# Kernel tuning notes

Measured on AMD Instinct MI355X. Metric: run time of the kernel, lower is better.

## Reference

```python
import jax, jax.numpy as jnp
import numpy as np

TOPK = 6
E = 512
IN = 384
M = 8192
LN_EPS = 1e-5


def _lin(x, w, b):
    # torch nn.Linear: y = x @ W^T + b, W is [out, in]
    return x @ w.T + b


def setup_inputs() -> dict:
    key = jax.random.key(0)
    ks = jax.random.split(key, 16)
    s = lambda k, sh: (jax.random.normal(k, sh, dtype=jnp.float32) * 0.02)
    return {
        "x": jax.random.normal(ks[0], (1, M, IN), dtype=jnp.float32),
        "fc1_w": s(ks[1], (E, IN)), "fc1_b": jnp.zeros((E,), jnp.float32),
        "wh_w": s(ks[2], (E, E)),   "wh_b": jnp.zeros((E,), jnp.float32),
        "wt_w": s(ks[3], (E, E)),   "wt_b": jnp.zeros((E,), jnp.float32),
        "l1_w": s(ks[4], (E, E)),   "l1_b": jnp.zeros((E,), jnp.float32),
        "l2_w": s(ks[5], (E, E)),   "l2_b": jnp.zeros((E,), jnp.float32),
        "a1_w": s(ks[6], (E // 2, E)), "a1_b": jnp.zeros((E // 2,), jnp.float32),
        "a2_w": s(ks[7], (1, E // 2)), "a2_b": jnp.zeros((1,), jnp.float32),
        "ln_g": jnp.ones((E,), jnp.float32), "ln_b": jnp.zeros((E,), jnp.float32),
    }


def reference(x, fc1_w, fc1_b, wh_w, wh_b, wt_w, wt_b,
              l1_w, l1_b, l2_w, l2_b, a1_w, a1_b, a2_w, a2_b, ln_g, ln_b):
    lrelu = jax.nn.leaky_relu  # slope 0.01 == torch default
    h = lrelu(_lin(x, fc1_w, fc1_b))                      # [B,M,E]
    h = (h + h.mean(axis=1, keepdims=True)) * 0.5
    e_h = _lin(h, wh_w, wh_b)                             # [B,M,E]
    e_t = _lin(h, wt_w, wt_b)                             # [B,M,E]
    scale = E ** (-0.5)
    attn_logit = (e_h * scale) @ jnp.swapaxes(e_t, -2, -1)  # [B,M,M]
    topk_weight, topk_index = jax.lax.top_k(attn_logit, TOPK)  # [B,M,K]
    # gather top-k neighbor tail embeddings: [B,M,K,E]
    Nb_h = jax.vmap(lambda et, idx: et[idx])(e_t, topk_index)
    topk_prob = jax.nn.softmax(topk_weight, axis=2)       # [B,M,K]
    eh_r = topk_prob[..., None] * Nb_h + (1.0 - topk_prob)[..., None] * e_h[:, :, None, :]
    gate = jnp.tanh(e_h[:, :, None, :] + eh_r)            # [B,M,K,E]
    # faithful to torch einsum('ijkl,ijkm->ijk'): sums l and m independently
    ka_weight = Nb_h.sum(axis=-1) * gate.sum(axis=-1)     # [B,M,K]
    ka_prob = jax.nn.softmax(ka_weight, axis=2)           # [B,M,K]
    e_Nh = jnp.einsum('bmk,bmke->bme', ka_prob, Nb_h)     # [B,M,E]
    sum_emb = lrelu(_lin(e_h + e_Nh, l1_w, l1_b))
    bi_emb = lrelu(_lin(e_h * e_Nh, l2_w, l2_b))
    emb = sum_emb + bi_emb                                # [B,M,E] (dropout = eval identity)
    hn = emb[0]                                           # squeeze(0) -> [M,E]
    # GeoGlobalAttention readout: gate_nn = Linear->LeakyReLU->Linear, softmax over nodes
    g = _lin(lrelu(_lin(hn, a1_w, a1_b)), a2_w, a2_b)     # [M,1]
    att = jax.nn.softmax(g, axis=0)
    pooled = (att * hn).sum(axis=0, keepdims=True)        # [1,E]
    mu = pooled.mean(axis=-1, keepdims=True)
    var = jnp.mean((pooled - mu) ** 2, axis=-1, keepdims=True)
    out = (pooled - mu) / jnp.sqrt(var + LN_EPS) * ln_g + ln_b
    return out
```

## Files before the change

### kernel.cpp

```cpp
#include <hip/hip_runtime.h>
#include <math.h>
#include <stdint.h>

#define M_NODES 8192
#define E_DIM   512
#define NTOPK   6
#define ATTN_SCALE 0.04419417382415922f
#define NEG_BIG (-1e38f)
#define CAND_CAP 192

typedef __attribute__((ext_vector_type(8))) short short8;
typedef __attribute__((ext_vector_type(4))) float f32x4;

__device__ __forceinline__ float lrelu(float v) { return v > 0.f ? v : 0.01f * v; }

__device__ __forceinline__ unsigned short f2bf(float f) {
  uint32_t u = __float_as_uint(f);
  uint32_t r = (u + 0x7FFFu + ((u >> 16) & 1u)) >> 16;
  return (unsigned short)r;
}
__device__ __forceinline__ float bf2f(unsigned short s) {
  return __uint_as_float(((uint32_t)s) << 16);
}

__device__ __forceinline__ void async_cp16(const void* gptr, void* lds) {
  auto g1 = reinterpret_cast<const __attribute__((address_space(1))) unsigned int*>(
      reinterpret_cast<uintptr_t>(gptr));
  auto l3 = reinterpret_cast<__attribute__((address_space(3))) unsigned int*>(
      reinterpret_cast<uintptr_t>(lds));
  __builtin_amdgcn_global_load_lds(g1, l3, 16, 0, 0);
}



__global__ __launch_bounds__(256) void wcast_kernel(
    const float* __restrict__ x, const float* __restrict__ fc1w,
    const float* __restrict__ whw, const float* __restrict__ wtw,
    const float* __restrict__ l1w, const float* __restrict__ l2w,
    const float* __restrict__ a1w,
    unsigned short* __restrict__ xT, unsigned short* __restrict__ fc1T,
    unsigned short* __restrict__ whT, unsigned short* __restrict__ wtT,
    unsigned short* __restrict__ l1T, unsigned short* __restrict__ l2T,
    unsigned short* __restrict__ a1T)
{
  const int gid = blockIdx.x * 256 + threadIdx.x;
  const float* src; unsigned short* dst; int K8, local;
  if (gid < 417792) {
    K8 = 48;
    if (gid < 393216) { src = x; dst = xT; local = gid; }
    else { src = fc1w; dst = fc1T; local = gid - 393216; }
  } else {
    K8 = 64;
    if (gid < 450560)      { src = whw; dst = whT; local = gid - 417792; }
    else if (gid < 483328) { src = wtw; dst = wtT; local = gid - 450560; }
    else if (gid < 516096) { src = l1w; dst = l1T; local = gid - 483328; }
    else if (gid < 548864) { src = l2w; dst = l2T; local = gid - 516096; }
    else                   { src = a1w; dst = a1T; local = gid - 548864; }
  }
  const int m = local / K8;
  const int k8 = local - m * K8;
  const float* p = src + (size_t)m * (K8 * 8) + k8 * 8;
  float4 v0 = ((const float4*)p)[0];
  float4 v1 = ((const float4*)p)[1];
  const int Kt = K8 >> 2;
  const size_t ti = ((size_t)(m >> 4) * Kt + (k8 >> 2)) * 512 + ((m & 15) + 16 * (k8 & 3)) * 8;
  uint4 pk;
  pk.x = (uint32_t)f2bf(v0.x) | ((uint32_t)f2bf(v0.y) << 16);
  pk.y = (uint32_t)f2bf(v0.z) | ((uint32_t)f2bf(v0.w) << 16);
  pk.z = (uint32_t)f2bf(v1.x) | ((uint32_t)f2bf(v1.y) << 16);
  pk.w = (uint32_t)f2bf(v1.z) | ((uint32_t)f2bf(v1.w) << 16);
  *(uint4*)(dst + ti) = pk;
}

__global__ __launch_bounds__(256, 4) void gemm1_kernel(
    const unsigned short* __restrict__ xT, const unsigned short* __restrict__ fc1T,
    const float* __restrict__ b1, unsigned short* __restrict__ hT,
    float* __restrict__ colsum)
{
  __shared__ unsigned short As[8 * 512];
  __shared__ unsigned short Bs[8 * 512];
  const int tid = threadIdx.x, lane = tid & 63, w = tid >> 6;
  const int wr = w >> 1, wc = w & 1;
  const int m0 = blockIdx.y * 128;
  const int n0 = blockIdx.x * 128;

  f32x4 acc[4][4];
#pragma unroll
  for (int i = 0; i < 4; i++)
#pragma unroll
    for (int j = 0; j < 4; j++) acc[i][j] = (f32x4){0.f, 0.f, 0.f, 0.f};

  for (int kt = 0; kt < 12; kt++) {
    const int s0 = w, s1 = w + 4;
    async_cp16(xT + ((size_t)((m0 >> 4) + s0) * 12 + kt) * 512 + lane * 8, &As[s0 * 512]);
    async_cp16(xT + ((size_t)((m0 >> 4) + s1) * 12 + kt) * 512 + lane * 8, &As[s1 * 512]);
    async_cp16(fc1T + ((size_t)((n0 >> 4) + s0) * 12 + kt) * 512 + lane * 8, &Bs[s0 * 512]);
    async_cp16(fc1T + ((size_t)((n0 >> 4) + s1) * 12 + kt) * 512 + lane * 8, &Bs[s1 * 512]);
    __syncthreads();
    short8 a[4], b[4];
#pragma unroll
    for (int i = 0; i < 4; i++) a[i] = *(const short8*)&As[(wr * 4 + i) * 512 + lane * 8];
#pragma unroll
    for (int j = 0; j < 4; j++) b[j] = *(const short8*)&Bs[(wc * 4 + j) * 512 + lane * 8];
#pragma unroll
    for (int i = 0; i < 4; i++)
#pragma unroll
      for (int j = 0; j < 4; j++)
        acc[i][j] = __builtin_amdgcn_mfma_f32_16x16x32_bf16(a[i], b[j], acc[i][j], 0, 0, 0);
    __syncthreads();
  }

  const int q = lane >> 4, lcol = lane & 15;
  float colp[4] = {};
#pragma unroll
  for (int i = 0; i < 4; i++)
#pragma unroll
    for (int j = 0; j < 4; j++) {
      const int c = n0 + wc * 64 + j * 16 + lcol;
      const float bias = b1[c];
#pragma unroll
      for (int d = 0; d < 4; d++) {
        const int r = m0 + wr * 64 + i * 16 + q * 4 + d;
        const float v = 0.5f * lrelu(acc[i][j][d] + bias);
        hT[((size_t)(r >> 4) * 16 + (c >> 5)) * 512 +
           ((r & 15) + 16 * ((c >> 3) & 3)) * 8 + (c & 7)] = f2bf(v);
        colp[j] += v;
      }
    }
#pragma unroll
  for (int j = 0; j < 4; j++) {
    colp[j] += __shfl_xor(colp[j], 16);
    colp[j] += __shfl_xor(colp[j], 32);
  }
  if (lane < 16) {
#pragma unroll
    for (int j = 0; j < 4; j++)
      atomicAdd(&colsum[n0 + wc * 64 + j * 16 + lcol], colp[j]);
  }
}

__global__ __launch_bounds__(256) void meanproj_kernel(
    const float* __restrict__ colsum, const float* __restrict__ whw,
    const float* __restrict__ wtw, const float* __restrict__ whb,
    const float* __restrict__ wtb, float* __restrict__ biasHT)
{
  const int lane = threadIdx.x & 63;
  const int c1024 = blockIdx.x * 4 + (threadIdx.x >> 6);
  const bool isH = c1024 < 512;
  const int c = isH ? c1024 : c1024 - 512;
  const float* W = (isH ? whw : wtw) + (size_t)c * 512 + lane * 8;
  const float* cs = colsum + lane * 8;
  float s = 0.f;
#pragma unroll
  for (int e = 0; e < 8; e++) s = fmaf(cs[e], W[e], s);
#pragma unroll
  for (int off = 32; off; off >>= 1) s += __shfl_xor(s, off);
  if (lane == 0)
    biasHT[c1024] = (isH ? whb : wtb)[c] + s * (1.f / (float)M_NODES);
}

__global__ __launch_bounds__(256, 4) void dual_gemm(
    const unsigned short* __restrict__ hT, const unsigned short* __restrict__ wstackT,
    const float* __restrict__ biasHT,
    unsigned short* __restrict__ ehT, unsigned short* __restrict__ etT,
    unsigned short* __restrict__ ehRow, unsigned short* __restrict__ etRow)
{
  __shared__ unsigned short As[8 * 512];
  __shared__ unsigned short Bs[8 * 512];
  const int tid = threadIdx.x, lane = tid & 63, w = tid >> 6;
  const int wr = w >> 1, wc = w & 1;
  const int m0 = blockIdx.y * 128;
  const int n0 = blockIdx.x * 128;

  f32x4 acc[4][4];
#pragma unroll
  for (int i = 0; i < 4; i++)
#pragma unroll
    for (int j = 0; j < 4; j++) acc[i][j] = (f32x4){0.f, 0.f, 0.f, 0.f};

  for (int kt = 0; kt < 16; kt++) {
    const int s0 = w, s1 = w + 4;
    async_cp16(hT + ((size_t)((m0 >> 4) + s0) * 16 + kt) * 512 + lane * 8, &As[s0 * 512]);
    async_cp16(hT + ((size_t)((m0 >> 4) + s1) * 16 + kt) * 512 + lane * 8, &As[s1 * 512]);
    async_cp16(wstackT + ((size_t)((n0 >> 4) + s0) * 16 + kt) * 512 + lane * 8, &Bs[s0 * 512]);
    async_cp16(wstackT + ((size_t)((n0 >> 4) + s1) * 16 + kt) * 512 + lane * 8, &Bs[s1 * 512]);
    __syncthreads();
    short8 a[4], b[4];
#pragma unroll
    for (int i = 0; i < 4; i++) a[i] = *(const short8*)&As[(wr * 4 + i) * 512 + lane * 8];
#pragma unroll
    for (int j = 0; j < 4; j++) b[j] = *(const short8*)&Bs[(wc * 4 + j) * 512 + lane * 8];
#pragma unroll
    for (int i = 0; i < 4; i++)
#pragma unroll
      for (int j = 0; j < 4; j++)
        acc[i][j] = __builtin_amdgcn_mfma_f32_16x16x32_bf16(a[i], b[j], acc[i][j], 0, 0, 0);
    __syncthreads();
  }

  const int q = lane >> 4, lcol = lane & 15;
  const bool isH = (n0 < 512);
  const int cb = isH ? n0 : (n0 - 512);
  unsigned short* T = isH ? ehT : etT;
  unsigned short* R = isH ? ehRow : etRow;

#pragma unroll
  for (int i = 0; i < 4; i++)
#pragma unroll
    for (int j = 0; j < 4; j++) {
      const int cl = wc * 64 + j * 16 + lcol;
      const float bias = biasHT[n0 + cl];
      const int c = cb + cl;
#pragma unroll
      for (int d = 0; d < 4; d++) {
        const int r = m0 + wr * 64 + i * 16 + q * 4 + d;
        const unsigned short us = f2bf(acc[i][j][d] + bias);
        T[((size_t)(r >> 4) * 16 + (c >> 5)) * 512 +
          ((r & 15) + 16 * ((c >> 3) & 3)) * 8 + (c & 7)] = us;
        R[(size_t)r * E_DIM + c] = us;
      }
    }
}

template <int MODE>
__global__ __launch_bounds__(256) void mfma_gemm(
    const unsigned short* __restrict__ At1, const unsigned short* __restrict__ At2,
    const unsigned short* __restrict__ Wt1, const unsigned short* __restrict__ Wt2,
    const float* __restrict__ b1, const float* __restrict__ b2,
    float* __restrict__ Cf, unsigned short* __restrict__ T1,
    unsigned short* __restrict__ Cbf, int N, int K)
{
  constexpr bool DUALW = (MODE == 2);
  __shared__ unsigned short As[2][8 * 512];
  __shared__ unsigned short Bs[2][4 * 512];
  const int Kt = K >> 5;
  const int tid = threadIdx.x, lane = tid & 63, w = tid >> 6;
  const int m0 = blockIdx.y * 128, n0 = blockIdx.x * 64;

  f32x4 acc0[2][4], acc1[2][4];
#pragma unroll
  for (int p = 0; p < 2; p++)
#pragma unroll
    for (int j = 0; j < 4; j++) {
      acc0[p][j] = (f32x4){0.f, 0.f, 0.f, 0.f};
      acc1[p][j] = (f32x4){0.f, 0.f, 0.f, 0.f};
    }

  for (int kt = 0; kt < Kt; kt++) {
    const unsigned short* a1p = At1 + ((size_t)((m0 >> 4) + 2 * w) * Kt + kt) * 512 + lane * 8;
    async_cp16(a1p, &As[0][(2 * w) * 512]);
    async_cp16(a1p + (size_t)Kt * 512, &As[0][(2 * w + 1) * 512]);
    if (MODE == 2) {
      const unsigned short* a2p = At2 + ((size_t)((m0 >> 4) + 2 * w) * Kt + kt) * 512 + lane * 8;
      async_cp16(a2p, &As[1][(2 * w) * 512]);
      async_cp16(a2p + (size_t)Kt * 512, &As[1][(2 * w + 1) * 512]);
    }
    const unsigned short* bp1 = Wt1 + ((size_t)((n0 >> 4) + w) * Kt + kt) * 512 + lane * 8;
    async_cp16(bp1, &Bs[0][w * 512]);
    if (DUALW) {
      const unsigned short* bp2 = Wt2 + ((size_t)((n0 >> 4) + w) * Kt + kt) * 512 + lane * 8;
      async_cp16(bp2, &Bs[1][w * 512]);
    }
    __syncthreads();
    short8 a[2], a2[2], bb[4], bb2[4];
#pragma unroll
    for (int p = 0; p < 2; p++) a[p] = *(const short8*)&As[0][(2 * w + p) * 512 + lane * 8];
    if (MODE == 2) {
#pragma unroll
      for (int p = 0; p < 2; p++) a2[p] = *(const short8*)&As[1][(2 * w + p) * 512 + lane * 8];
    }
#pragma unroll
    for (int j = 0; j < 4; j++) bb[j] = *(const short8*)&Bs[0][j * 512 + lane * 8];
    if (DUALW) {
#pragma unroll
      for (int j = 0; j < 4; j++) bb2[j] = *(const short8*)&Bs[1][j * 512 + lane * 8];
    }
#pragma unroll
    for (int p = 0; p < 2; p++)
#pragma unroll
      for (int j = 0; j < 4; j++) {
        acc0[p][j] = __builtin_amdgcn_mfma_f32_16x16x32_bf16(a[p], bb[j], acc0[p][j], 0, 0, 0);
        if (MODE == 2)
          acc1[p][j] = __builtin_amdgcn_mfma_f32_16x16x32_bf16(a2[p], bb2[j], acc1[p][j], 0, 0, 0);
      }
    __syncthreads();
  }

  const int lrow = (lane >> 4) * 4, lcol = lane & 15;

  if (MODE == 3) {
    float part[2][4] = {};
#pragma unroll
    for (int p = 0; p < 2; p++)
#pragma unroll
      for (int j = 0; j < 4; j++) {
        const int c = n0 + j * 16 + lcol;
        const float bias1 = b1[c];
        const float w2 = b2[c];
#pragma unroll
        for (int d = 0; d < 4; d++)
          part[p][d] = fmaf(lrelu(acc0[p][j][d] + bias1), w2, part[p][d]);
      }
#pragma unroll
    for (int p = 0; p < 2; p++)
#pragma unroll
      for (int d = 0; d < 4; d++) {
#pragma unroll
        for (int off = 1; off < 16; off <<= 1)
          part[p][d] += __shfl_xor(part[p][d], off);
      }
    if (lcol == 0) {
#pragma unroll
      for (int p = 0; p < 2; p++)
#pragma unroll
        for (int d = 0; d < 4; d++)
          atomicAdd(&Cf[m0 + w * 32 + p * 16 + lrow + d], part[p][d]);
    }
    return;
  }

  const int NT = N >> 5;
#pragma unroll
  for (int p = 0; p < 2; p++)
#pragma unroll
    for (int j = 0; j < 4; j++) {
      const int c = n0 + j * 16 + lcol;
      const float bias1 = b1[c];
      const float bias2 = b2[c];
#pragma unroll
      for (int d = 0; d < 4; d++) {
        const int r = m0 + w * 32 + p * 16 + lrow + d;
        const float e = lrelu(acc0[p][j][d] + bias1) + lrelu(acc1[p][j][d] + bias2);
        T1[((size_t)(r >> 4) * NT + (c >> 5)) * 512 +
           ((r & 15) + 16 * ((c >> 3) & 3)) * 8 + (c & 7)] = f2bf(e);
        Cbf[(size_t)r * N + c] = f2bf(e);
      }
    }
}

__global__ __launch_bounds__(256, 4) void sgemm_kernel(
    const unsigned short* __restrict__ ehT, const unsigned short* __restrict__ etT,
    unsigned short* __restrict__ sc, float* __restrict__ tmax)
{
  __shared__ unsigned short As[8 * 512];
  __shared__ unsigned short Bs[8 * 512];
  const int tid = threadIdx.x, lane = tid & 63, w = tid >> 6;
  const int wr = w >> 1, wc = w & 1;
  const int m0 = blockIdx.y * 128;
  const int n0 = blockIdx.x * 128;

  f32x4 acc[4][4];
#pragma unroll
  for (int i = 0; i < 4; i++)
#pragma unroll
    for (int j = 0; j < 4; j++) acc[i][j] = (f32x4){0.f, 0.f, 0.f, 0.f};

  for (int kt = 0; kt < 16; kt++) {
    const int s0 = w, s1 = w + 4;
    async_cp16(ehT + ((size_t)((m0 >> 4) + s0) * 16 + kt) * 512 + lane * 8, &As[s0 * 512]);
    async_cp16(ehT + ((size_t)((m0 >> 4) + s1) * 16 + kt) * 512 + lane * 8, &As[s1 * 512]);
    async_cp16(etT + ((size_t)((n0 >> 4) + s0) * 16 + kt) * 512 + lane * 8, &Bs[s0 * 512]);
    async_cp16(etT + ((size_t)((n0 >> 4) + s1) * 16 + kt) * 512 + lane * 8, &Bs[s1 * 512]);
    __syncthreads();
    short8 a[4], b[4];
#pragma unroll
    for (int i = 0; i < 4; i++) a[i] = *(const short8*)&As[(wr * 4 + i) * 512 + lane * 8];
#pragma unroll
    for (int j = 0; j < 4; j++) b[j] = *(const short8*)&Bs[(wc * 4 + j) * 512 + lane * 8];
#pragma unroll
    for (int i = 0; i < 4; i++)
#pragma unroll
      for (int j = 0; j < 4; j++)
        acc[i][j] = __builtin_amdgcn_mfma_f32_16x16x32_bf16(a[i], b[j], acc[i][j], 0, 0, 0);
    __syncthreads();
  }

  const int q = lane >> 4, lcol = lane & 15;
  const int bn = blockIdx.x;

  float rm[4][4];
#pragma unroll
  for (int i = 0; i < 4; i++)
#pragma unroll
    for (int d = 0; d < 4; d++) rm[i][d] = NEG_BIG;

#pragma unroll
  for (int i = 0; i < 4; i++)
#pragma unroll
    for (int d = 0; d < 4; d++) {
      unsigned short o[4];
#pragma unroll
      for (int j = 0; j < 4; j++) {
        o[j] = f2bf(acc[i][j][d]);
        rm[i][d] = fmaxf(rm[i][d], bf2f(o[j]));
      }
      const int row = m0 + wr * 64 + i * 16 + q * 4 + d;
      const size_t off = ((size_t)row * 64 + bn) * 128 + (wc * 16 + lcol) * 4;
      *(uint2*)(sc + off) = *(uint2*)o;
    }

#pragma unroll
  for (int i = 0; i < 4; i++)
#pragma unroll
    for (int d = 0; d < 4; d++) {
#pragma unroll
      for (int off = 1; off < 16; off <<= 1)
        rm[i][d] = fmaxf(rm[i][d], __shfl_xor(rm[i][d], off));
    }

  if (lcol == 0) {
#pragma unroll
    for (int i = 0; i < 4; i++)
#pragma unroll
      for (int d = 0; d < 4; d++)
        tmax[(size_t)(m0 + wr * 64 + i * 16 + q * 4 + d) * 128 +
             bn * 2 + wc] = rm[i][d];
  }
}

__global__ __launch_bounds__(256) void scan_combine_kernel(
    const unsigned short* __restrict__ sc, const float* __restrict__ tmax,
    const unsigned short* __restrict__ ehRow, const unsigned short* __restrict__ etRow,
    unsigned short* __restrict__ s1T, unsigned short* __restrict__ s2T)
{
  __shared__ float cv[4][CAND_CAP];
  __shared__ int   ci[4][CAND_CAP];
  __shared__ int   cnt[4];
  __shared__ float t6v[4][8];
  __shared__ int   t6i[4][8];
  const int tid = threadIdx.x;
  const int lane = tid & 63;
  const int w = tid >> 6;
  const int row = blockIdx.x * 4 + w;

  if (lane == 0) cnt[w] = 0;
  if (lane < 8) { t6v[w][lane] = 0.f; t6i[w][lane] = 0; }

  const float* tm = tmax + (size_t)row * 128;
  const float v2 = fmaxf(tm[lane], tm[lane + 64]);
  const float bmax = fmaxf(tm[2 * lane], tm[2 * lane + 1]);
  uint32_t u = __float_as_uint(v2);
  u = ((int)u >= 0) ? (u | 0x80000000u) : ~u;
  uint32_t key = (u & ~63u) | (uint32_t)lane;
  float tau = 0.f;
#pragma unroll
  for (int it = 0; it < 6; it++) {
    uint32_t k = key;
#pragma unroll
    for (int off = 32; off; off >>= 1) {
      const uint32_t o = (uint32_t)__shfl_xor((int)k, off);
      k = k > o ? k : o;
    }
    const int wl = (int)(k & 63u);
    if (it == 5) tau = __shfl(v2, wl);
    if (lane == wl) key = 0u;
  }

  unsigned long long mask = __ballot(bmax >= tau);
  const unsigned short* rp = sc + (size_t)row * 8192;
  while (mask) {
    const int bn = __ffsll(mask) - 1;
    mask &= mask - 1;
    const uint32_t uu = *(const uint32_t*)(rp + bn * 128 + lane * 2);
    const float f0 = bf2f((unsigned short)(uu & 0xFFFFu));
    const float f1 = bf2f((unsigned short)(uu >> 16));
#pragma unroll
    for (int e = 0; e < 2; e++) {
      const float f = e ? f1 : f0;
      if (f >= tau) {
        const int idx128 = lane * 2 + e;
        const int g = idx128 >> 2, j = idx128 & 3;
        const int col = bn * 128 + (g >> 4) * 64 + j * 16 + (g & 15);
        const int slot = atomicAdd(&cnt[w], 1);
        if (slot < CAND_CAP) { cv[w][slot] = f; ci[w][slot] = col; }
      }
    }
  }
  __syncthreads();

  int n = cnt[w];
  n = n < CAND_CAP ? n : CAND_CAP;
  for (int c = lane; c < n; c += 64) {
    const float v = cv[w][c];
    const int idx = ci[w][c];
    int rank = 0;
    for (int j = 0; j < n; j++) {
      const float vj = cv[w][j];
      rank += (vj > v) || (vj == v && ci[w][j] < idx);
    }
    if (rank < NTOPK) { t6v[w][rank] = v; t6i[w][rank] = idx; }
  }
  __syncthreads();

  const int m = row;
  float wv[NTOPK]; int id[NTOPK];
#pragma unroll
  for (int k = 0; k < NTOPK; k++) {
    wv[k] = t6v[w][k] * ATTN_SCALE;
    id[k] = t6i[w][k];
  }

  float mx = wv[0];
#pragma unroll
  for (int k = 1; k < NTOPK; k++) mx = fmaxf(mx, wv[k]);
  float p[NTOPK]; float s = 0.f;
#pragma unroll
  for (int k = 0; k < NTOPK; k++) { p[k] = expf(wv[k] - mx); s += p[k]; }
  const float inv = 1.f / s;
#pragma unroll
  for (int k = 0; k < NTOPK; k++) p[k] *= inv;

  short8 eh8 = *(const short8*)(ehRow + (size_t)m * E_DIM + lane * 8);
  float ehv[8];
#pragma unroll
  for (int e = 0; e < 8; e++) ehv[e] = bf2f((unsigned short)eh8[e]);

  float nv[NTOPK][8];
#pragma unroll
  for (int k = 0; k < NTOPK; k++) {
    short8 nb = *(const short8*)(etRow + (size_t)id[k] * E_DIM + lane * 8);
#pragma unroll
    for (int e = 0; e < 8; e++) nv[k][e] = bf2f((unsigned short)nb[e]);
  }

  float ka[NTOPK];
#pragma unroll
  for (int k = 0; k < NTOPK; k++) {
    float snb = 0.f, sg = 0.f;
    const float aa = 2.f - p[k], bb = p[k];
#pragma unroll
    for (int e = 0; e < 8; e++) {
      snb += nv[k][e];
      sg += tanhf(fmaf(aa, ehv[e], bb * nv[k][e]));
    }
#pragma unroll
    for (int off = 32; off; off >>= 1) {
      snb += __shfl_xor(snb, off);
      sg += __shfl_xor(sg, off);
    }
    ka[k] = snb * sg;
  }
  float km = ka[0];
#pragma unroll
  for (int k = 1; k < NTOPK; k++) km = fmaxf(km, ka[k]);
  float kp[NTOPK]; float ks = 0.f;
#pragma unroll
  for (int k = 0; k < NTOPK; k++) { kp[k] = expf(ka[k] - km); ks += kp[k]; }
  const float kinv = 1.f / ks;

  const size_t tbase = ((size_t)(m >> 4) * 16 + (lane >> 2)) * 512 +
                       ((m & 15) + 16 * (lane & 3)) * 8;
  unsigned short o1[8], o2[8];
#pragma unroll
  for (int e = 0; e < 8; e++) {
    float o = 0.f;
#pragma unroll
    for (int k = 0; k < NTOPK; k++) o = fmaf(kp[k], nv[k][e], o);
    o *= kinv;
    o1[e] = f2bf(ehv[e] + o);
    o2[e] = f2bf(ehv[e] * o);
  }
  *(short8*)(s1T + tbase) = *(short8*)o1;
  *(short8*)(s2T + tbase) = *(short8*)o2;
}

__global__ __launch_bounds__(256) void pooled_kernel(
    const unsigned short* __restrict__ emb, const float* __restrict__ g,
    float* __restrict__ pooled, float* __restrict__ wsum)
{
  const int t = threadIdx.x;
  const int r0 = blockIdx.x * 128;
  float a0 = 0.f, a1 = 0.f, lsum = 0.f;
  for (int r = 0; r < 128; r++) {
    const int m = r0 + r;
    const float wv = expf(g[m]);
    lsum += wv;
    a0 = fmaf(wv, bf2f(emb[(size_t)m * E_DIM + t]), a0);
    a1 = fmaf(wv, bf2f(emb[(size_t)m * E_DIM + 256 + t]), a1);
  }
  atomicAdd(&pooled[t], a0);
  atomicAdd(&pooled[t + 256], a1);
  if (t == 0) atomicAdd(wsum, lsum);
}

__global__ __launch_bounds__(512) void ln_kernel(
    const float* __restrict__ pooled, const float* __restrict__ wsum,
    const float* __restrict__ lng, const float* __restrict__ lnb,
    float* __restrict__ out)
{
  __shared__ float red[8];
  __shared__ float red2[8];
  const int t = threadIdx.x;
  const float v = pooled[t] / wsum[0];
  float s = v;
#pragma unroll
  for (int off = 32; off; off >>= 1) s += __shfl_xor(s, off);
  if ((t & 63) == 0) red[t >> 6] = s;
  __syncthreads();
  float tot = 0.f;
  for (int i = 0; i < 8; i++) tot += red[i];
  const float mu = tot / (float)E_DIM;
  const float d = v - mu;
  float q = d * d;
#pragma unroll
  for (int off = 32; off; off >>= 1) q += __shfl_xor(q, off);
  if ((t & 63) == 0) red2[t >> 6] = q;
  __syncthreads();
  float vt = 0.f;
  for (int i = 0; i < 8; i++) vt += red2[i];
  const float var = vt / (float)E_DIM;
  out[t] = d * rsqrtf(var + 1e-5f) * lng[t] + lnb[t];
}

extern "C" void kernel_launch(void* const* d_in, const int* in_sizes, int n_in,
                              void* d_out, int out_size, void* d_ws, size_t ws_size,
                              hipStream_t stream)
{
  const float* x     = (const float*)d_in[0];
  const float* fc1_w = (const float*)d_in[1];
  const float* fc1_b = (const float*)d_in[2];
  const float* wh_w  = (const float*)d_in[3];
  const float* wh_b  = (const float*)d_in[4];
  const float* wt_w  = (const float*)d_in[5];
  const float* wt_b  = (const float*)d_in[6];
  const float* l1_w  = (const float*)d_in[7];
  const float* l1_b  = (const float*)d_in[8];
  const float* l2_w  = (const float*)d_in[9];
  const float* l2_b  = (const float*)d_in[10];
  const float* a1_w  = (const float*)d_in[11];
  const float* a1_b  = (const float*)d_in[12];
  const float* a2_w  = (const float*)d_in[13];
  const float* a2_b  = (const float*)d_in[14];
  const float* ln_g  = (const float*)d_in[15];
  const float* ln_b  = (const float*)d_in[16];
  (void)a2_b;

  char* ws = (char*)d_ws;
  const size_t MiB = 1 << 20;
  unsigned short* fc1T = (unsigned short*)(ws + 0);
  unsigned short* whT  = (unsigned short*)(ws + 393216);
  unsigned short* wtT  = (unsigned short*)(ws + 917504);
  unsigned short* l1T  = (unsigned short*)(ws + 1441792);
  unsigned short* l2T  = (unsigned short*)(ws + 1966080);
  unsigned short* a1T  = (unsigned short*)(ws + 2490368);
  unsigned short* xT     = (unsigned short*)(ws + 3 * MiB);
  unsigned short* hT     = (unsigned short*)(ws + 25 * MiB);
  unsigned short* ehT    = (unsigned short*)(ws + 33 * MiB);
  unsigned short* etT    = (unsigned short*)(ws + 41 * MiB);
  unsigned short* ehRow  = (unsigned short*)(ws + 49 * MiB);
  unsigned short* etRow  = (unsigned short*)(ws + 57 * MiB);
  float*          tmaxb  = (float*)(ws + 65 * MiB);
  unsigned short* s1T    = (unsigned short*)(ws + 3 * MiB);
  unsigned short* s2T    = (unsigned short*)(ws + 11 * MiB);
  unsigned short* embT   = (unsigned short*)(ws + 19 * MiB);
  unsigned short* embRow = (unsigned short*)(ws + 27 * MiB);
  unsigned short* scores = (unsigned short*)(ws + 96 * MiB);
  char*           smal   = ws + 69 * MiB;
  float* colsum = (float*)(smal);
  float* biasHT = (float*)(smal + 2048);
  float* g      = (float*)(smal + 8192);
  float* stats  = (float*)(smal + 40960);
  float* pooled = (float*)(smal + 45056);

  hipMemsetAsync(smal, 0, 47104, stream);

  wcast_kernel<<<2208, 256, 0, stream>>>(x, fc1_w, wh_w, wt_w, l1_w, l2_w, a1_w,
                                         xT, fc1T, whT, wtT, l1T, l2T, a1T);
  gemm1_kernel<<<dim3(4, 64), 256, 0, stream>>>(xT, fc1T, fc1_b, hT, colsum);
  meanproj_kernel<<<256, 256, 0, stream>>>(colsum, wh_w, wt_w, wh_b, wt_b, biasHT);
  dual_gemm<<<dim3(8, 64), 256, 0, stream>>>(hT, whT, biasHT, ehT, etT, ehRow, etRow);
  sgemm_kernel<<<dim3(64, 64), 256, 0, stream>>>(ehT, etT, scores, tmaxb);
  scan_combine_kernel<<<M_NODES / 4, 256, 0, stream>>>(
      scores, tmaxb, ehRow, etRow, s1T, s2T);
  mfma_gemm<2><<<dim3(8, 64), 256, 0, stream>>>(
      s1T, s2T, l1T, l2T, l1_b, l2_b, nullptr, embT, embRow, 512, 512);
  mfma_gemm<3><<<dim3(4, 64), 256, 0, stream>>>(
      embT, nullptr, a1T, nullptr, a1_b, a2_w, g, nullptr, nullptr, 256, 512);
  pooled_kernel<<<64, 256, 0, stream>>>(embRow, g, pooled, stats);
  ln_kernel<<<1, 512, 0, stream>>>(pooled, stats, ln_g, ln_b, (float*)d_out);
}
```

Before: 296.5 us.

## Enlarge score GEMM tile to 256x256 with double-buffered LDS and setprio

The M×M score GEMM now uses 256x256 block tiles with 8 waves instead of 128x128 with 4 waves, and a K step of 64 rather than 32. The next K-tile is prefetched asynchronously into a second LDS buffer while the current one is consumed. The MFMA issue is split into quadrant phases, each wrapped in s_setprio and separated by barriers. The aim is to reduce global and LDS traffic per FLOP and hide load latency, at the cost of higher register and LDS use (128 KB per block), which limits occupancy.

```diff
diff --git a/kernel.cpp b/kernel.cpp
--- a/kernel.cpp
+++ b/kernel.cpp
@@ -338,83 +338,147 @@
     }
 }
 
-__global__ __launch_bounds__(256, 4) void sgemm_kernel(
+__global__ __launch_bounds__(512, 2) void sgemm_kernel(
     const unsigned short* __restrict__ ehT, const unsigned short* __restrict__ etT,
     unsigned short* __restrict__ sc, float* __restrict__ tmax)
 {
-  __shared__ unsigned short As[8 * 512];
-  __shared__ unsigned short Bs[8 * 512];
+  __shared__ unsigned short As[2][32 * 512];
+  __shared__ unsigned short Bs[2][32 * 512];
   const int tid = threadIdx.x, lane = tid & 63, w = tid >> 6;
-  const int wr = w >> 1, wc = w & 1;
-  const int m0 = blockIdx.y * 128;
-  const int n0 = blockIdx.x * 128;
-
-  f32x4 acc[4][4];
-#pragma unroll
-  for (int i = 0; i < 4; i++)
+  const int wr = w >> 2, wc = w & 3;
+  const int m0 = blockIdx.y * 256;
+  const int n0 = blockIdx.x * 256;
+
+  f32x4 acc[8][4];
+#pragma unroll
+  for (int i = 0; i < 8; i++)
 #pragma unroll
     for (int j = 0; j < 4; j++) acc[i][j] = (f32x4){0.f, 0.f, 0.f, 0.f};
 
-  for (int kt = 0; kt < 16; kt++) {
-    const int s0 = w, s1 = w + 4;
-    async_cp16(ehT + ((size_t)((m0 >> 4) + s0) * 16 + kt) * 512 + lane * 8, &As[s0 * 512]);
-    async_cp16(ehT + ((size_t)((m0 >> 4) + s1) * 16 + kt) * 512 + lane * 8, &As[s1 * 512]);
-    async_cp16(etT + ((size_t)((n0 >> 4) + s0) * 16 + kt) * 512 + lane * 8, &Bs[s0 * 512]);
-    async_cp16(etT + ((size_t)((n0 >> 4) + s1) * 16 + kt) * 512 + lane * 8, &Bs[s1 * 512]);
+  auto stage = [&](int kt, int bsel) {
+#pragma unroll
+    for (int r = 0; r < 8; r++) {
+      const int c = r * 8 + w;
+      if (c < 32) {
+        async_cp16(ehT + ((size_t)((m0 >> 4) + (c >> 1)) * 16 + (kt * 2 + (c & 1))) * 512 + lane * 8,
+                   &As[bsel][c * 512]);
+      } else {
+        const int c2 = c - 32;
+        async_cp16(etT + ((size_t)((n0 >> 4) + (c2 >> 1)) * 16 + (kt * 2 + (c2 & 1))) * 512 + lane * 8,
+                   &Bs[bsel][c2 * 512]);
+      }
+    }
+  };
+
+  stage(0, 0);
+
+  short8 af[8], bf[8];
+  for (int kt = 0; kt < 8; kt++) {
+    const int cur = kt & 1;
     __syncthreads();
-    short8 a[4], b[4];
-#pragma unroll
-    for (int i = 0; i < 4; i++) a[i] = *(const short8*)&As[(wr * 4 + i) * 512 + lane * 8];
-#pragma unroll
-    for (int j = 0; j < 4; j++) b[j] = *(const short8*)&Bs[(wc * 4 + j) * 512 + lane * 8];
-#pragma unroll
-    for (int i = 0; i < 4; i++)
-#pragma unroll
-      for (int j = 0; j < 4; j++)
-        acc[i][j] = __builtin_amdgcn_mfma_f32_16x16x32_bf16(a[i], b[j], acc[i][j], 0, 0, 0);
-    __syncthreads();
+    if (kt < 7) stage(kt + 1, cur ^ 1);
+
+#pragma unroll
+    for (int ii = 0; ii < 4; ii++)
+#pragma unroll
+      for (int ks = 0; ks < 2; ks++)
+        af[ii * 2 + ks] = *(const short8*)&As[cur][((wr * 8 + ii) * 2 + ks) * 512 + lane * 8];
+#pragma unroll
+    for (int jj = 0; jj < 2; jj++)
+#pragma unroll
+      for (int ks = 0; ks < 2; ks++)
+        bf[jj * 2 + ks] = *(const short8*)&Bs[cur][((wc * 4 + jj) * 2 + ks) * 512 + lane * 8];
+    __builtin_amdgcn_s_setprio(1);
+#pragma unroll
+    for (int ii = 0; ii < 4; ii++)
+#pragma unroll
+      for (int jj = 0; jj < 2; jj++)
+#pragma unroll
+        for (int ks = 0; ks < 2; ks++)
+          acc[ii][jj] = __builtin_amdgcn_mfma_f32_16x16x32_bf16(
+              af[ii * 2 + ks], bf[jj * 2 + ks], acc[ii][jj], 0, 0, 0);
+    __builtin_amdgcn_s_setprio(0);
+    __builtin_amdgcn_s_barrier();
+
+#pragma unroll
+    for (int jj = 2; jj < 4; jj++)
+#pragma unroll
+      for (int ks = 0; ks < 2; ks++)
+        bf[jj * 2 + ks] = *(const short8*)&Bs[cur][((wc * 4 + jj) * 2 + ks) * 512 + lane * 8];
+    __builtin_amdgcn_s_setprio(1);
+#pragma unroll
+    for (int ii = 0; ii < 4; ii++)
+#pragma unroll
+      for (int jj = 2; jj < 4; jj++)
+#pragma unroll
+        for (int ks = 0; ks < 2; ks++)
+          acc[ii][jj] = __builtin_amdgcn_mfma_f32_16x16x32_bf16(
+              af[ii * 2 + ks], bf[jj * 2 + ks], acc[ii][jj], 0, 0, 0);
+    __builtin_amdgcn_s_setprio(0);
+    __builtin_amdgcn_s_barrier();
+
+#pragma unroll
+    for (int ii = 0; ii < 4; ii++)
+#pragma unroll
+      for (int ks = 0; ks < 2; ks++)
+        af[ii * 2 + ks] = *(const short8*)&As[cur][((wr * 8 + 4 + ii) * 2 + ks) * 512 + lane * 8];
+    __builtin_amdgcn_s_setprio(1);
+#pragma unroll
+    for (int ii = 0; ii < 4; ii++)
+#pragma unroll
+      for (int jj = 2; jj < 4; jj++)
+#pragma unroll
+        for (int ks = 0; ks < 2; ks++)
+          acc[4 + ii][jj] = __builtin_amdgcn_mfma_f32_16x16x32_bf16(
+              af[ii * 2 + ks], bf[jj * 2 + ks], acc[4 + ii][jj], 0, 0, 0);
+    __builtin_amdgcn_s_setprio(0);
+    __builtin_amdgcn_s_barrier();
+
+    __builtin_amdgcn_s_setprio(1);
+#pragma unroll
+    for (int ii = 0; ii < 4; ii++)
+#pragma unroll
+      for (int jj = 0; jj < 2; jj++)
+#pragma unroll
+        for (int ks = 0; ks < 2; ks++)
+          acc[4 + ii][jj] = __builtin_amdgcn_mfma_f32_16x16x32_bf16(
+              af[ii * 2 + ks], bf[jj * 2 + ks], acc[4 + ii][jj], 0, 0, 0);
+    __builtin_amdgcn_s_setprio(0);
   }
 
   const int q = lane >> 4, lcol = lane & 15;
-  const int bn = blockIdx.x;
-
-  float rm[4][4];
-#pragma unroll
-  for (int i = 0; i < 4; i++)
-#pragma unroll
-    for (int d = 0; d < 4; d++) rm[i][d] = NEG_BIG;
-
-#pragma unroll
-  for (int i = 0; i < 4; i++)
+  const int bn = blockIdx.x * 2 + (wc >> 1);
+  const int wcS = wc & 1;
+
+#pragma unroll
+  for (int i = 0; i < 8; i++) {
+    float rm[4];
+#pragma unroll
+    for (int d = 0; d < 4; d++) rm[d] = NEG_BIG;
 #pragma unroll
     for (int d = 0; d < 4; d++) {
       unsigned short o[4];
 #pragma unroll
       for (int j = 0; j < 4; j++) {
         o[j] = f2bf(acc[i][j][d]);
-        rm[i][d] = fmaxf(rm[i][d], bf2f(o[j]));
-      }
-      const int row = m0 + wr * 64 + i * 16 + q * 4 + d;
-      const size_t off = ((size_t)row * 64 + bn) * 128 + (wc * 16 + lcol) * 4;
+        rm[d] = fmaxf(rm[d], bf2f(o[j]));
+      }
+      const int row = m0 + wr * 128 + i * 16 + q * 4 + d;
+      const size_t off = ((size_t)row * 64 + bn) * 128 + (wcS * 16 + lcol) * 4;
       *(uint2*)(sc + off) = *(uint2*)o;
     }
-
-#pragma unroll
-  for (int i = 0; i < 4; i++)
 #pragma unroll
     for (int d = 0; d < 4; d++) {
 #pragma unroll
-      for (int off = 1; off < 16; off <<= 1)
-        rm[i][d] = fmaxf(rm[i][d], __shfl_xor(rm[i][d], off));
-    }
-
-  if (lcol == 0) {
-#pragma unroll
-    for (int i = 0; i < 4; i++)
+      for (int off2 = 1; off2 < 16; off2 <<= 1)
+        rm[d] = fmaxf(rm[d], __shfl_xor(rm[d], off2));
+    }
+    if (lcol == 0) {
 #pragma unroll
       for (int d = 0; d < 4; d++)
-        tmax[(size_t)(m0 + wr * 64 + i * 16 + q * 4 + d) * 128 +
-             bn * 2 + wc] = rm[i][d];
+        tmax[(size_t)(m0 + wr * 128 + i * 16 + q * 4 + d) * 128 +
+             blockIdx.x * 4 + wc] = rm[d];
+    }
   }
 }
 
@@ -669,7 +733,7 @@
   gemm1_kernel<<<dim3(4, 64), 256, 0, stream>>>(xT, fc1T, fc1_b, hT, colsum);
   meanproj_kernel<<<256, 256, 0, stream>>>(colsum, wh_w, wt_w, wh_b, wt_b, biasHT);
   dual_gemm<<<dim3(8, 64), 256, 0, stream>>>(hT, whT, biasHT, ehT, etT, ehRow, etRow);
-  sgemm_kernel<<<dim3(64, 64), 256, 0, stream>>>(ehT, etT, scores, tmaxb);
+  sgemm_kernel<<<dim3(32, 32), 512, 0, stream>>>(ehT, etT, scores, tmaxb);
   scan_combine_kernel<<<M_NODES / 4, 256, 0, stream>>>(
       scores, tmaxb, ehRow, etRow, s1T, s2T);
   mfma_gemm<2><<<dim3(8, 64), 256, 0, stream>>>(
```

New measurement: 299.2 us. No clear change (+0.9%).

## Compute per-segment top-6 in score GEMM epilogue instead of writing full scores

Applied to the files above, without the earlier changes.

The score GEMM epilogue no longer writes the full 8192x8192 bf16 score matrix and per-tile maxima. Each 64-column segment now reduces to its top-6 packed keys (order-preserving bf16 value plus inverted column index) with wave shuffles, and stores only those. The combine kernel merges the 128 sorted segment lists per row with a wave-wide argmax loop, replacing the threshold scan, LDS candidate buffer and rank sort. This removes about 128 MB of score traffic, at the cost of six shuffle-reduction rounds per output row in the GEMM epilogue.

```diff
diff --git a/kernel.cpp b/kernel.cpp
--- a/kernel.cpp
+++ b/kernel.cpp
@@ -6,8 +6,7 @@
 #define E_DIM   512
 #define NTOPK   6
 #define ATTN_SCALE 0.04419417382415922f
-#define NEG_BIG (-1e38f)
-#define CAND_CAP 192
+#define CAND_SEGS 128
 
 typedef __attribute__((ext_vector_type(8))) short short8;
 typedef __attribute__((ext_vector_type(4))) float f32x4;
@@ -340,7 +339,7 @@
 
 __global__ __launch_bounds__(256, 4) void sgemm_kernel(
     const unsigned short* __restrict__ ehT, const unsigned short* __restrict__ etT,
-    unsigned short* __restrict__ sc, float* __restrict__ tmax)
+    uint32_t* __restrict__ cand)
 {
   __shared__ unsigned short As[8 * 512];
   __shared__ unsigned short Bs[8 * 512];
@@ -376,128 +375,86 @@
   }
 
   const int q = lane >> 4, lcol = lane & 15;
-  const int bn = blockIdx.x;
-
-  float rm[4][4];
+  const int seg = blockIdx.x * 2 + wc;
+
 #pragma unroll
   for (int i = 0; i < 4; i++)
 #pragma unroll
-    for (int d = 0; d < 4; d++) rm[i][d] = NEG_BIG;
-
-#pragma unroll
-  for (int i = 0; i < 4; i++)
-#pragma unroll
     for (int d = 0; d < 4; d++) {
-      unsigned short o[4];
+      uint32_t kb[4];
 #pragma unroll
       for (int j = 0; j < 4; j++) {
-        o[j] = f2bf(acc[i][j][d]);
-        rm[i][d] = fmaxf(rm[i][d], bf2f(o[j]));
-      }
-      const int row = m0 + wr * 64 + i * 16 + q * 4 + d;
-      const size_t off = ((size_t)row * 64 + bn) * 128 + (wc * 16 + lcol) * 4;
-      *(uint2*)(sc + off) = *(uint2*)o;
-    }
-
-#pragma unroll
-  for (int i = 0; i < 4; i++)
-#pragma unroll
-    for (int d = 0; d < 4; d++) {
-#pragma unroll
-      for (int off = 1; off < 16; off <<= 1)
-        rm[i][d] = fmaxf(rm[i][d], __shfl_xor(rm[i][d], off));
-    }
-
-  if (lcol == 0) {
-#pragma unroll
-    for (int i = 0; i < 4; i++)
-#pragma unroll
-      for (int d = 0; d < 4; d++)
-        tmax[(size_t)(m0 + wr * 64 + i * 16 + q * 4 + d) * 128 +
-             bn * 2 + wc] = rm[i][d];
-  }
-}
-
-__global__ __launch_bounds__(256) void scan_combine_kernel(
-    const unsigned short* __restrict__ sc, const float* __restrict__ tmax,
+        const int col = n0 + wc * 64 + j * 16 + lcol;
+        const uint32_t ub = ((uint32_t)f2bf(acc[i][j][d])) << 16;
+        const uint32_t ob = ((int)ub >= 0) ? (ub | 0x80000000u) : ~ub;
+        kb[j] = (ob & 0xFFFF0000u) | (uint32_t)(8191 - col);
+      }
+      uint32_t sel[6];
+#pragma unroll
+      for (int t = 0; t < 6; t++) {
+        uint32_t m01 = kb[0] > kb[1] ? kb[0] : kb[1];
+        uint32_t m23 = kb[2] > kb[3] ? kb[2] : kb[3];
+        uint32_t m = m01 > m23 ? m01 : m23;
+#pragma unroll
+        for (int off = 1; off < 16; off <<= 1) {
+          const uint32_t o = (uint32_t)__shfl_xor((int)m, off);
+          m = m > o ? m : o;
+        }
+        sel[t] = m;
+#pragma unroll
+        for (int j = 0; j < 4; j++)
+          if (kb[j] == m) kb[j] = 0u;
+      }
+      if (lcol == 0) {
+        const int row = m0 + wr * 64 + i * 16 + q * 4 + d;
+        uint32_t* cp = cand + ((size_t)row * CAND_SEGS + seg) * 6;
+        uint2 u01; u01.x = sel[0]; u01.y = sel[1];
+        uint2 u23; u23.x = sel[2]; u23.y = sel[3];
+        uint2 u45; u45.x = sel[4]; u45.y = sel[5];
+        ((uint2*)cp)[0] = u01;
+        ((uint2*)cp)[1] = u23;
+        ((uint2*)cp)[2] = u45;
+      }
+    }
+}
+
+__global__ __launch_bounds__(256) void combine_kernel(
+    const uint32_t* __restrict__ cand,
     const unsigned short* __restrict__ ehRow, const unsigned short* __restrict__ etRow,
     unsigned short* __restrict__ s1T, unsigned short* __restrict__ s2T)
 {
-  __shared__ float cv[4][CAND_CAP];
-  __shared__ int   ci[4][CAND_CAP];
-  __shared__ int   cnt[4];
-  __shared__ float t6v[4][8];
-  __shared__ int   t6i[4][8];
   const int tid = threadIdx.x;
   const int lane = tid & 63;
   const int w = tid >> 6;
   const int row = blockIdx.x * 4 + w;
-
-  if (lane == 0) cnt[w] = 0;
-  if (lane < 8) { t6v[w][lane] = 0.f; t6i[w][lane] = 0; }
-
-  const float* tm = tmax + (size_t)row * 128;
-  const float v2 = fmaxf(tm[lane], tm[lane + 64]);
-  const float bmax = fmaxf(tm[2 * lane], tm[2 * lane + 1]);
-  uint32_t u = __float_as_uint(v2);
-  u = ((int)u >= 0) ? (u | 0x80000000u) : ~u;
-  uint32_t key = (u & ~63u) | (uint32_t)lane;
-  float tau = 0.f;
-#pragma unroll
-  for (int it = 0; it < 6; it++) {
-    uint32_t k = key;
-#pragma unroll
-    for (int off = 32; off; off >>= 1) {
-      const uint32_t o = (uint32_t)__shfl_xor((int)k, off);
-      k = k > o ? k : o;
-    }
-    const int wl = (int)(k & 63u);
-    if (it == 5) tau = __shfl(v2, wl);
-    if (lane == wl) key = 0u;
-  }
-
-  unsigned long long mask = __ballot(bmax >= tau);
-  const unsigned short* rp = sc + (size_t)row * 8192;
-  while (mask) {
-    const int bn = __ffsll(mask) - 1;
-    mask &= mask - 1;
-    const uint32_t uu = *(const uint32_t*)(rp + bn * 128 + lane * 2);
-    const float f0 = bf2f((unsigned short)(uu & 0xFFFFu));
-    const float f1 = bf2f((unsigned short)(uu >> 16));
-#pragma unroll
-    for (int e = 0; e < 2; e++) {
-      const float f = e ? f1 : f0;
-      if (f >= tau) {
-        const int idx128 = lane * 2 + e;
-        const int g = idx128 >> 2, j = idx128 & 3;
-        const int col = bn * 128 + (g >> 4) * 64 + j * 16 + (g & 15);
-        const int slot = atomicAdd(&cnt[w], 1);
-        if (slot < CAND_CAP) { cv[w][slot] = f; ci[w][slot] = col; }
-      }
-    }
-  }
-  __syncthreads();
-
-  int n = cnt[w];
-  n = n < CAND_CAP ? n : CAND_CAP;
-  for (int c = lane; c < n; c += 64) {
-    const float v = cv[w][c];
-    const int idx = ci[w][c];
-    int rank = 0;
-    for (int j = 0; j < n; j++) {
-      const float vj = cv[w][j];
-      rank += (vj > v) || (vj == v && ci[w][j] < idx);
-    }
-    if (rank < NTOPK) { t6v[w][rank] = v; t6i[w][rank] = idx; }
-  }
-  __syncthreads();
-
   const int m = row;
+
+  const uint32_t* cp = cand + ((size_t)row * CAND_SEGS + 2 * lane) * 6;
+  const uint4 va = *(const uint4*)cp;
+  const uint4 vb = *(const uint4*)(cp + 4);
+  const uint4 vc = *(const uint4*)(cp + 8);
+  uint32_t a0 = va.x, a1 = va.y, a2 = va.z, a3 = va.w, a4 = vb.x, a5 = vb.y;
+  uint32_t b0 = vb.z, b1 = vb.w, b2 = vc.x, b3 = vc.y, b4 = vc.z, b5 = vc.w;
+
   float wv[NTOPK]; int id[NTOPK];
 #pragma unroll
-  for (int k = 0; k < NTOPK; k++) {
-    wv[k] = t6v[w][k] * ATTN_SCALE;
-    id[k] = t6i[w][k];
+  for (int t = 0; t < NTOPK; t++) {
+    const uint32_t best = a0 > b0 ? a0 : b0;
+    uint32_t mm = best;
+#pragma unroll
+    for (int off = 1; off < 64; off <<= 1) {
+      const uint32_t o = (uint32_t)__shfl_xor((int)mm, off);
+      mm = mm > o ? mm : o;
+    }
+    if (best == mm) {
+      if (a0 == mm) { a0 = a1; a1 = a2; a2 = a3; a3 = a4; a4 = a5; a5 = 0u; }
+      else          { b0 = b1; b1 = b2; b2 = b3; b3 = b4; b4 = b5; b5 = 0u; }
+    }
+    const uint32_t h = mm >> 16;
+    const uint32_t u = (h & 0x8000u) ? ((h & 0x7FFFu) << 16)
+                                     : ((~h & 0xFFFFu) << 16);
+    wv[t] = __uint_as_float(u) * ATTN_SCALE;
+    id[t] = 8191 - (int)(mm & 0x1FFFu);
   }
 
   float mx = wv[0];
@@ -649,12 +606,11 @@
   unsigned short* etT    = (unsigned short*)(ws + 41 * MiB);
   unsigned short* ehRow  = (unsigned short*)(ws + 49 * MiB);
   unsigned short* etRow  = (unsigned short*)(ws + 57 * MiB);
-  float*          tmaxb  = (float*)(ws + 65 * MiB);
   unsigned short* s1T    = (unsigned short*)(ws + 3 * MiB);
   unsigned short* s2T    = (unsigned short*)(ws + 11 * MiB);
   unsigned short* embT   = (unsigned short*)(ws + 19 * MiB);
   unsigned short* embRow = (unsigned short*)(ws + 27 * MiB);
-  unsigned short* scores = (unsigned short*)(ws + 96 * MiB);
+  uint32_t*       cand   = (uint32_t*)(ws + 96 * MiB);
   char*           smal   = ws + 69 * MiB;
   float* colsum = (float*)(smal);
   float* biasHT = (float*)(smal + 2048);
@@ -669,9 +625,8 @@
   gemm1_kernel<<<dim3(4, 64), 256, 0, stream>>>(xT, fc1T, fc1_b, hT, colsum);
   meanproj_kernel<<<256, 256, 0, stream>>>(colsum, wh_w, wt_w, wh_b, wt_b, biasHT);
   dual_gemm<<<dim3(8, 64), 256, 0, stream>>>(hT, whT, biasHT, ehT, etT, ehRow, etRow);
-  sgemm_kernel<<<dim3(64, 64), 256, 0, stream>>>(ehT, etT, scores, tmaxb);
-  scan_combine_kernel<<<M_NODES / 4, 256, 0, stream>>>(
-      scores, tmaxb, ehRow, etRow, s1T, s2T);
+  sgemm_kernel<<<dim3(64, 64), 256, 0, stream>>>(ehT, etT, cand);
+  combine_kernel<<<M_NODES / 4, 256, 0, stream>>>(cand, ehRow, etRow, s1T, s2T);
   mfma_gemm<2><<<dim3(8, 64), 256, 0, stream>>>(
       s1T, s2T, l1T, l2T, l1_b, l2_b, nullptr, embT, embRow, 512, 512);
   mfma_gemm<3><<<dim3(4, 64), 256, 0, stream>>>(
```

New measurement: 374.6 us. 1.26x slower.
